# Optimization experiments

Measured on AMD Instinct MI355X. Metric: run time of the kernel, lower is better.

The kernel has to match this reference:

```python
import jax, jax.numpy as jnp
import numpy as np

DIM = 256
HEADS = 8
KS = 3          # deform conv kernel size
N = KS * KS     # sampling points per output pixel
PAD = 1


def conv2d(x, w, b=None, stride=1, padding=0):
    out = jax.lax.conv_general_dilated(
        x, w, (stride, stride), [(padding, padding)] * 2,
        dimension_numbers=('NCHW', 'OIHW', 'NCHW'))
    if b is not None:
        out = out + b[None, :, None, None]
    return out


def deform_conv(x, w_pconv, b_pconv, w_dconv):
    b, c, h, w = x.shape
    offset = conv2d(x, w_pconv, b_pconv, padding=1)      # (b, 2N, h, w)
    off = offset.transpose(0, 2, 3, 1)                   # (b, h, w, 2N); [:N]=x-off, [N:]=y-off
    xp = jnp.pad(x, ((0, 0), (0, 0), (PAD, PAD), (PAD, PAD)))
    hp, wp = h + 2 * PAD, w + 2 * PAD
    r = jnp.arange(-(KS - 1) // 2, (KS - 1) // 2 + 1, dtype=x.dtype)
    pnx, pny = jnp.meshgrid(r, r, indexing='ij')
    # sampling positions, 1-indexed into the padded input (matches the torch ref)
    px = off[..., :N] + pnx.reshape(-1) + jnp.arange(1, h + 1, dtype=x.dtype)[None, :, None, None]
    py = off[..., N:] + pny.reshape(-1) + jnp.arange(1, w + 1, dtype=x.dtype)[None, None, :, None]
    fx = jnp.floor(px)
    fy = jnp.floor(py)
    qlt_x = jnp.clip(fx, 0, hp - 1)
    qlt_y = jnp.clip(fy, 0, wp - 1)
    qrb_x = jnp.clip(fx + 1, 0, hp - 1)
    qrb_y = jnp.clip(fy + 1, 0, wp - 1)
    pxc = jnp.clip(px, 0, hp - 1)
    pyc = jnp.clip(py, 0, wp - 1)
    # bilinear weights (can be negative at clamped borders, as in the torch ref)
    g_lt = (1 + (qlt_x - pxc)) * (1 + (qlt_y - pyc))
    g_rb = (1 - (qrb_x - pxc)) * (1 - (qrb_y - pyc))
    g_lb = (1 + (qlt_x - pxc)) * (1 - (qrb_y - pyc))
    g_rt = (1 - (qrb_x - pxc)) * (1 + (qlt_y - pyc))
    ilt_x = qlt_x.astype(jnp.int32)
    ilt_y = qlt_y.astype(jnp.int32)
    irb_x = qrb_x.astype(jnp.int32)
    irb_y = qrb_y.astype(jnp.int32)

    def gather(xb, ix, iy):
        return xb[:, ix, iy]                              # (c, h, w, N)

    gat = jax.vmap(gather)
    x_lt = gat(xp, ilt_x, ilt_y)
    x_rb = gat(xp, irb_x, irb_y)
    x_lb = gat(xp, ilt_x, irb_y)
    x_rt = gat(xp, irb_x, ilt_y)
    x_off = (g_lt[:, None] * x_lt + g_rb[:, None] * x_rb
             + g_lb[:, None] * x_lb + g_rt[:, None] * x_rt)   # (b, c, h, w, N)
    # 'b c h w (i j) -> b c (h i) (w j)' then ks-strided conv
    x_off = x_off.reshape(b, c, h, w, KS, KS).transpose(0, 1, 2, 4, 3, 5)
    x_off = x_off.reshape(b, c, h * KS, w * KS)
    return conv2d(x_off, w_dconv, None, stride=KS)


def ssa_forward(x, w_pconv, b_pconv, w_dconv, w_qkv, temperature, w_proj):
    b, c, h, w = x.shape
    hw = h * w
    ch = c // HEADS
    q = deform_conv(x, w_pconv, b_pconv, w_dconv)         # (b, c, h, w)
    qkv = jnp.einsum('bchw,oc->bohw', x, w_qkv)           # 1x1 conv, (b, 3c, h, w)
    k = qkv[:, c:2 * c]
    v = qkv[:, 2 * c:]
    q = q.reshape(b, HEADS, ch, hw)
    k = k.reshape(b, HEADS, ch, hw)
    v = v.reshape(b, HEADS, ch, hw)
    k = k / jnp.maximum(jnp.linalg.norm(k, axis=-1, keepdims=True), 1e-12)
    v = v / jnp.maximum(jnp.linalg.norm(v, axis=-1, keepdims=True), 1e-12)
    attn = jnp.einsum('bhcn,bhdn->bhcd', q, k) * temperature[None]   # (b, h, ch, ch)
    attn = jax.nn.softmax(attn, axis=-1)
    out = jnp.einsum('bhcd,bhdn->bhcn', attn, v).reshape(b, c, h, w)
    return jnp.einsum('bchw,oc->bohw', out, w_proj)       # project_out 1x1


def setup_inputs() -> dict:
    key = jax.random.key(0)
    ks = jax.random.split(key, 6)
    B, H, W = 2, 96, 96
    x = jax.random.normal(ks[0], (B, DIM, H, W), jnp.float32)
    w_pconv = jax.random.normal(ks[1], (2 * N, DIM, KS, KS), jnp.float32) * 0.01
    b_pconv = jax.random.normal(ks[2], (2 * N,), jnp.float32) * 0.01
    w_dconv = jax.random.normal(ks[3], (DIM, DIM, KS, KS), jnp.float32) * 0.02
    w_qkv = jax.random.normal(ks[4], (3 * DIM, DIM), jnp.float32) * 0.05
    temperature = jnp.ones((HEADS, 1, 1), jnp.float32)
    w_proj = jax.random.normal(ks[5], (DIM, DIM), jnp.float32) * 0.05
    return dict(x=x, w_pconv=w_pconv, b_pconv=b_pconv, w_dconv=w_dconv,
                w_qkv=w_qkv, temperature=temperature, w_proj=w_proj)


def reference(x, w_pconv, b_pconv, w_dconv, w_qkv, temperature, w_proj):
    return ssa_forward(x, w_pconv, b_pconv, w_dconv, w_qkv, temperature, w_proj)
```

## Files before the change

### kernel.cpp

```cpp
#include <hip/hip_runtime.h>
#include <math.h>

#define BB 2
#define CC 256
#define HW 96
#define PP 9216
#define KO 18
#define HEADS 8
#define NCH 18

typedef short bf16x8 __attribute__((ext_vector_type(8)));
typedef float f32x4 __attribute__((ext_vector_type(4)));

#define NP_O    0UL
#define W2_O    147456UL
#define IDX_O   331776UL
#define WGT_O   995328UL
#define WT2_O   1658880UL
#define WP2_O   2248704UL
#define WQ2_O   2322432UL
#define QP_O    2584576UL
#define KV_O    12021760UL
#define AP_O    21459968UL

__device__ __forceinline__ ushort f2bf_rne(float f) {
    unsigned u = __float_as_uint(f);
    unsigned r = (u + 0x7FFFu + ((u >> 16) & 1u)) >> 16;
    return (ushort)r;
}
__device__ __forceinline__ float bf2f(ushort h) {
    return __uint_as_float(((unsigned)h) << 16);
}

__global__ __launch_bounds__(256) void k_prep_wt(const float* __restrict__ wd,
                                                 ushort* __restrict__ h,
                                                 ushort* __restrict__ lo) {
    int tid = blockIdx.x * 256 + threadIdx.x;
    if (tid >= 9 * 8 * 1024 * 8) return;
    int e = tid & 7;
    int u = (tid >> 3) & 1023;
    int cs = (tid >> 13) & 7;
    int kk = tid >> 16;
    int oh = u >> 6, rem = u & 63;
    int lrow = rem & 15, lhi = rem >> 4;
    int o = oh * 16 + lrow;
    int c = cs * 32 + lhi * 8 + e;
    float v = wd[o * 2304 + c * 9 + kk];
    ushort hh = f2bf_rne(v);
    h[tid] = hh;
    lo[tid] = f2bf_rne(v - bf2f(hh));
}

__global__ __launch_bounds__(256) void k_prep_wp(const float* __restrict__ wp,
                                                 ushort* __restrict__ h,
                                                 ushort* __restrict__ lo) {
    int tid = blockIdx.x * 256 + threadIdx.x;
    if (tid >= 9 * 8 * 128 * 8) return;
    int e = tid & 7;
    int u = (tid >> 3) & 127;
    int cs = (tid >> 10) & 7;
    int kk = tid >> 13;
    int mf = u >> 6, rem = u & 63;
    int lrow = rem & 15, lhi = rem >> 4;
    int o = mf * 16 + lrow;
    int c = cs * 32 + lhi * 8 + e;
    float v = (o < KO) ? wp[(o * 256 + c) * 9 + kk] : 0.f;
    ushort hh = f2bf_rne(v);
    h[tid] = hh;
    lo[tid] = f2bf_rne(v - bf2f(hh));
}

__global__ __launch_bounds__(256) void k_prep_w(const float* __restrict__ W,
                                                ushort* __restrict__ h,
                                                ushort* __restrict__ lo,
                                                int total) {
    int tid = blockIdx.x * 256 + threadIdx.x;
    if (tid >= total) return;
    int e = tid & 7;
    int u = (tid >> 3) & 1023;
    int csg = (tid >> 13) & 7;
    int mt = tid >> 16;
    int rem = u & 63;
    int lrow = rem & 15, lhi = rem >> 4;
    int o = mt * 256 + (u >> 6) * 16 + lrow;
    int c = csg * 32 + lhi * 8 + e;
    float v = W[o * 256 + c];
    ushort hh = f2bf_rne(v);
    h[tid] = hh;
    lo[tid] = f2bf_rne(v - bf2f(hh));
}

__global__ __launch_bounds__(256) void k_pconv(const float* __restrict__ x,
                                               const ushort* __restrict__ wp2h,
                                               const ushort* __restrict__ wp2l,
                                               float* __restrict__ ppart) {
    int s = blockIdx.x;
    int xcd = s & 7;
    int b = xcd & 1, ks = xcd >> 1;
    int p0 = (s >> 3) * 64;
    int t = threadIdx.x;
    int l = t & 63, w = t >> 6;
    int lrow = l & 15, lhi = l >> 4;
    int p = t & 63, cg = t >> 6;
    __shared__ __align__(16) ushort Sh[64 * 40];
    __shared__ __align__(16) ushort Sl[64 * 40];
    f32x4 acc[2];
    acc[0] = (f32x4)0.f; acc[1] = (f32x4)0.f;
    const float* xb = x + (size_t)b * CC * PP;
    int pix = p0 + p;
    int i_ = pix / 96, j_ = pix % 96;
#pragma unroll 1
    for (int cs = 0; cs < 2; ++cs) {
        int csg = ks * 2 + cs;
        const float* xc0 = xb + (size_t)(csg * 32 + cg * 8) * PP;
#pragma unroll 1
        for (int kk = 0; kk < 9; ++kk) {
            int di = kk / 3 - 1, dj = kk % 3 - 1;
            bool vOK = ((unsigned)(i_ + di) < 96u) && ((unsigned)(j_ + dj) < 96u);
            int poff = pix + di * 96 + dj;
            __syncthreads();
            bf16x8 ah[2], al[2];
#pragma unroll
            for (int mf = 0; mf < 2; ++mf) {
                size_t gi = (((size_t)(kk * 8 + csg)) * 128 + (mf * 64 + l)) * 8;
                ah[mf] = *(const bf16x8*)&wp2h[gi];
                al[mf] = *(const bf16x8*)&wp2l[gi];
            }
            bf16x8 vh, vl;
#pragma unroll
            for (int i = 0; i < 8; ++i) {
                float v = vOK ? xc0[(size_t)i * PP + poff] : 0.f;
                ushort hh = f2bf_rne(v);
                vh[i] = (short)hh;
                vl[i] = (short)f2bf_rne(v - bf2f(hh));
            }
            *(bf16x8*)&Sh[p * 40 + cg * 8] = vh;
            *(bf16x8*)&Sl[p * 40 + cg * 8] = vl;
            __syncthreads();
            bf16x8 Bh = *(const bf16x8*)&Sh[(w * 16 + lrow) * 40 + lhi * 8];
            bf16x8 Bl = *(const bf16x8*)&Sl[(w * 16 + lrow) * 40 + lhi * 8];
#pragma unroll
            for (int mf = 0; mf < 2; ++mf) {
                acc[mf] = __builtin_amdgcn_mfma_f32_16x16x32_bf16(ah[mf], Bh, acc[mf], 0, 0, 0);
                acc[mf] = __builtin_amdgcn_mfma_f32_16x16x32_bf16(ah[mf], Bl, acc[mf], 0, 0, 0);
                acc[mf] = __builtin_amdgcn_mfma_f32_16x16x32_bf16(al[mf], Bh, acc[mf], 0, 0, 0);
            }
        }
    }
    float* pr = ppart + ((size_t)(ks * BB + b) * 32) * PP;
#pragma unroll
    for (int mf = 0; mf < 2; ++mf)
#pragma unroll
        for (int j = 0; j < 4; ++j)
            pr[(size_t)(mf * 16 + lhi * 4 + j) * PP + p0 + w * 16 + lrow] = acc[mf][j];
}

__global__ __launch_bounds__(256) void k_bilin2(const float* __restrict__ pp,
                                                const float* __restrict__ bp,
                                                int4* __restrict__ idx4,
                                                float4* __restrict__ wgt4) {
    int idx = blockIdx.x * 256 + threadIdx.x;
    if (idx >= BB * 9 * PP) return;
    int p = idx % PP;
    int bn = idx / PP;
    int n = bn % 9, b = bn / 9;
    int i = p / 96, j = p % 96;
    float ox = bp[n], oy = bp[n + 9];
#pragma unroll
    for (int k = 0; k < 4; ++k) {
        ox += pp[((size_t)(k * BB + b) * 32 + n) * PP + p];
        oy += pp[((size_t)(k * BB + b) * 32 + n + 9) * PP + p];
    }
    float px = ox + (float)(n / 3 - 1) + (float)(i + 1);
    float py = oy + (float)(n % 3 - 1) + (float)(j + 1);
    float fx = floorf(px), fy = floorf(py);
    float qltx = fminf(fmaxf(fx, 0.f), 97.f);
    float qlty = fminf(fmaxf(fy, 0.f), 97.f);
    float qrbx = fminf(fmaxf(fx + 1.f, 0.f), 97.f);
    float qrby = fminf(fmaxf(fy + 1.f, 0.f), 97.f);
    float pxc = fminf(fmaxf(px, 0.f), 97.f);
    float pyc = fminf(fmaxf(py, 0.f), 97.f);
    float glt = (1.f + (qltx - pxc)) * (1.f + (qlty - pyc));
    float grb = (1.f - (qrbx - pxc)) * (1.f - (qrby - pyc));
    float glb = (1.f + (qltx - pxc)) * (1.f - (qrby - pyc));
    float grt = (1.f - (qrbx - pxc)) * (1.f + (qlty - pyc));
    int x0 = (int)qltx - 1, y0 = (int)qlty - 1;
    int x1 = (int)qrbx - 1, y1 = (int)qrby - 1;
    bool vlt = (x0 >= 0 && x0 < 96 && y0 >= 0 && y0 < 96);
    bool vrb = (x1 >= 0 && x1 < 96 && y1 >= 0 && y1 < 96);
    bool vlb = (x0 >= 0 && x0 < 96 && y1 >= 0 && y1 < 96);
    bool vrt = (x1 >= 0 && x1 < 96 && y0 >= 0 && y0 < 96);
    int4 id;
    id.x = vlt ? x0 * 96 + y0 : 0;
    id.y = vrb ? x1 * 96 + y1 : 0;
    id.z = vlb ? x0 * 96 + y1 : 0;
    id.w = vrt ? x1 * 96 + y0 : 0;
    idx4[idx] = id;
    wgt4[idx] = make_float4(vlt ? glt : 0.f, vrb ? grb : 0.f,
                            vlb ? glb : 0.f, vrt ? grt : 0.f);
}

__global__ __launch_bounds__(256) void k_dconv(const float* __restrict__ x,
                                               const ushort* __restrict__ wt2h,
                                               const ushort* __restrict__ wt2l,
                                               const int4* __restrict__ idx4,
                                               const float4* __restrict__ wgt4,
                                               float* __restrict__ qpart) {
    int s = blockIdx.x;
    int xcd = s & 7, ib = s >> 3;
    int combo = xcd >> 1;
    int b = combo & 1;
    int half = combo >> 1;
    int ptile = (xcd & 1) * 144 + ib;
    int p0 = ptile * 32;
    int t = threadIdx.x;
    int l = t & 63, w = t >> 6;
    int lrow = l & 15, lhi = l >> 4;
    int obase = w * 64;
    int pl = t & 31, cg = t >> 5;

    __shared__ __align__(16) ushort Sh0[32 * 40], Sl0[32 * 40];
    __shared__ __align__(16) ushort Sh1[32 * 40], Sl1[32 * 40];
    __shared__ int4 Tid[9 * 32];
    __shared__ float4 Twg[9 * 32];

    for (int e = t; e < 9 * 32; e += 256) {
        int kk = e >> 5, pq = e & 31;
        size_t tb = ((size_t)b * 9 + kk) * PP + p0 + pq;
        Tid[e] = idx4[tb];
        Twg[e] = wgt4[tb];
    }

    f32x4 acc[4][2];
#pragma unroll
    for (int mf = 0; mf < 4; ++mf)
#pragma unroll
        for (int nf = 0; nf < 2; ++nf) acc[mf][nf] = (f32x4)0.f;

    const float* xb = x + (size_t)b * CC * PP;
    int h4 = half * 4;

    float R[16];
    float4 g4r;

    auto LD = [&](int i) {
        int cs = i / 9, kk = i % 9;
        int csg = h4 + cs;
        int4 id = Tid[kk * 32 + pl];
        g4r = Twg[kk * 32 + pl];
        const float* xp0 = xb + (size_t)(csg * 32 + cg * 4) * PP;
#pragma unroll
        for (int q = 0; q < 4; ++q) {
            const float* xc = xp0 + (size_t)q * PP;
            R[q * 4 + 0] = xc[id.x];
            R[q * 4 + 1] = xc[id.y];
            R[q * 4 + 2] = xc[id.z];
            R[q * 4 + 3] = xc[id.w];
        }
    };
    auto CONV = [&](ushort* Sh, ushort* Sl) {
        ushort4 vh, vl;
#pragma unroll
        for (int q = 0; q < 4; ++q) {
            float v = g4r.x * R[q * 4 + 0];
            v = fmaf(g4r.y, R[q * 4 + 1], v);
            v = fmaf(g4r.z, R[q * 4 + 2], v);
            v = fmaf(g4r.w, R[q * 4 + 3], v);
            ushort hh = f2bf_rne(v);
            ushort ll = f2bf_rne(v - bf2f(hh));
            if (q == 0)      { vh.x = hh; vl.x = ll; }
            else if (q == 1) { vh.y = hh; vl.y = ll; }
            else if (q == 2) { vh.z = hh; vl.z = ll; }
            else             { vh.w = hh; vl.w = ll; }
        }
        *(ushort4*)&Sh[pl * 40 + cg * 4] = vh;
        *(ushort4*)&Sl[pl * 40 + cg * 4] = vl;
    };
    auto COMPUTE = [&](int i, const ushort* Sh, const ushort* Sl) {
        int cs = i / 9, kk = i % 9;
        int csg = h4 + cs;
        bf16x8 ah[4], al[4];
#pragma unroll
        for (int mf = 0; mf < 4; ++mf) {
            size_t gi = (((size_t)(kk * 8 + csg)) * 1024 + ((w * 4 + mf) * 64 + l)) * 8;
            ah[mf] = *(const bf16x8*)&wt2h[gi];
            al[mf] = *(const bf16x8*)&wt2l[gi];
        }
        bf16x8 Bh2[2], Bl2[2];
#pragma unroll
        for (int nf = 0; nf < 2; ++nf) {
            Bh2[nf] = *(const bf16x8*)&Sh[(nf * 16 + lrow) * 40 + lhi * 8];
            Bl2[nf] = *(const bf16x8*)&Sl[(nf * 16 + lrow) * 40 + lhi * 8];
        }
        __builtin_amdgcn_s_setprio(1);
#pragma unroll
        for (int mf = 0; mf < 4; ++mf)
#pragma unroll
            for (int nf = 0; nf < 2; ++nf) {
                acc[mf][nf] = __builtin_amdgcn_mfma_f32_16x16x32_bf16(ah[mf], Bh2[nf], acc[mf][nf], 0, 0, 0);
                acc[mf][nf] = __builtin_amdgcn_mfma_f32_16x16x32_bf16(ah[mf], Bl2[nf], acc[mf][nf], 0, 0, 0);
                acc[mf][nf] = __builtin_amdgcn_mfma_f32_16x16x32_bf16(al[mf], Bh2[nf], acc[mf][nf], 0, 0, 0);
            }
        __builtin_amdgcn_s_setprio(0);
    };

    __syncthreads();
    LD(0); CONV(Sh0, Sl0);
    LD(1);
    __syncthreads();

#pragma unroll 1
    for (int i0 = 0; i0 < 36; i0 += 2) {
        CONV(Sh1, Sl1);
        if (i0 + 2 < 36) LD(i0 + 2);
        COMPUTE(i0, Sh0, Sl0);
        __syncthreads();
        if (i0 + 2 < 36) CONV(Sh0, Sl0);
        if (i0 + 3 < 36) LD(i0 + 3);
        COMPUTE(i0 + 1, Sh1, Sl1);
        __syncthreads();
    }

    float* qh = qpart + (size_t)half * BB * CC * PP + (size_t)b * CC * PP;
#pragma unroll
    for (int mf = 0; mf < 4; ++mf)
#pragma unroll
        for (int nf = 0; nf < 2; ++nf)
#pragma unroll
            for (int j = 0; j < 4; ++j)
                qh[(size_t)(obase + mf * 16 + lhi * 4 + j) * PP + p0 + nf * 16 + lrow] =
                    acc[mf][nf][j];
}

__global__ __launch_bounds__(256) void k_gemm_bf(const float* __restrict__ Bsrc,
                                                 const ushort* __restrict__ A2h,
                                                 const ushort* __restrict__ A2l,
                                                 float* __restrict__ C,
                                                 int mtiles, int bRowStride, int bRowOff,
                                                 int aBatchStride,
                                                 float* __restrict__ npart) {
    int s = blockIdx.x;
    int xcd = s & 7, ib = s >> 3;
    int b, mt, ptile;
    if (mtiles == 2) {
        int combo = xcd >> 1;
        b = combo & 1; mt = combo >> 1;
        ptile = (xcd & 1) * 72 + ib;
    } else {
        b = xcd >> 2; mt = 0;
        ptile = (xcd & 3) * 36 + ib;
    }
    int p0 = ptile * 64;
    int t = threadIdx.x;
    int l = t & 63, w = t >> 6;
    int lrow = l & 15, lhi = l >> 4;
    int obase = w * 64;
    int p = t & 63, cg = t >> 6;
    __shared__ __align__(16) ushort Sh[64 * 40];
    __shared__ __align__(16) ushort Sl[64 * 40];
    f32x4 acc[4][4];
#pragma unroll
    for (int mf = 0; mf < 4; ++mf)
#pragma unroll
        for (int nf = 0; nf < 4; ++nf) acc[mf][nf] = (f32x4)0.f;
    const float* Bb = Bsrc + ((size_t)b * bRowStride + bRowOff) * PP;
    const ushort* Ah = A2h + (size_t)b * aBatchStride;
    const ushort* Al = A2l + (size_t)b * aBatchStride;
#pragma unroll 1
    for (int csg = 0; csg < 8; ++csg) {
        __syncthreads();
        bf16x8 ah[4], al[4];
#pragma unroll
        for (int mf = 0; mf < 4; ++mf) {
            size_t gi = (((size_t)(mt * 8 + csg)) * 1024 + ((w * 4 + mf) * 64 + l)) * 8;
            ah[mf] = *(const bf16x8*)&Ah[gi];
            al[mf] = *(const bf16x8*)&Al[gi];
        }
        const float* xr = Bb + (size_t)(csg * 32 + cg * 8) * PP + p0 + p;
        bf16x8 vh, vl;
#pragma unroll
        for (int i = 0; i < 8; ++i) {
            float v = xr[(size_t)i * PP];
            ushort hh = f2bf_rne(v);
            vh[i] = (short)hh;
            vl[i] = (short)f2bf_rne(v - bf2f(hh));
        }
        *(bf16x8*)&Sh[p * 40 + cg * 8] = vh;
        *(bf16x8*)&Sl[p * 40 + cg * 8] = vl;
        __syncthreads();
        bf16x8 Bh4[4], Bl4[4];
#pragma unroll
        for (int nf = 0; nf < 4; ++nf) {
            Bh4[nf] = *(const bf16x8*)&Sh[(nf * 16 + lrow) * 40 + lhi * 8];
            Bl4[nf] = *(const bf16x8*)&Sl[(nf * 16 + lrow) * 40 + lhi * 8];
        }
#pragma unroll
        for (int mf = 0; mf < 4; ++mf) {
#pragma unroll
            for (int nf = 0; nf < 4; ++nf) {
                acc[mf][nf] = __builtin_amdgcn_mfma_f32_16x16x32_bf16(ah[mf], Bh4[nf], acc[mf][nf], 0, 0, 0);
                acc[mf][nf] = __builtin_amdgcn_mfma_f32_16x16x32_bf16(ah[mf], Bl4[nf], acc[mf][nf], 0, 0, 0);
                acc[mf][nf] = __builtin_amdgcn_mfma_f32_16x16x32_bf16(al[mf], Bh4[nf], acc[mf][nf], 0, 0, 0);
            }
        }
    }
    float* Cb = C + (size_t)b * (mtiles * 256) * PP;
#pragma unroll
    for (int mf = 0; mf < 4; ++mf)
#pragma unroll
        for (int nf = 0; nf < 4; ++nf)
#pragma unroll
            for (int j = 0; j < 4; ++j)
                Cb[(size_t)(mt * 256 + obase + mf * 16 + lhi * 4 + j) * PP + p0 + nf * 16 + lrow] =
                    acc[mf][nf][j];
    if (npart) {
        float sq[4][4];
#pragma unroll
        for (int mf = 0; mf < 4; ++mf)
#pragma unroll
            for (int j = 0; j < 4; ++j) {
                float v0 = acc[mf][0][j], v1 = acc[mf][1][j];
                float v2 = acc[mf][2][j], v3 = acc[mf][3][j];
                sq[mf][j] = v0 * v0 + v1 * v1 + v2 * v2 + v3 * v3;
            }
#pragma unroll
        for (int m = 1; m <= 8; m <<= 1)
#pragma unroll
            for (int mf = 0; mf < 4; ++mf)
#pragma unroll
                for (int j = 0; j < 4; ++j)
                    sq[mf][j] += __shfl_xor(sq[mf][j], m, 64);
        if (lrow == 0) {
            float* np = npart + ((size_t)(b * 2 + mt) * 144 + ptile) * 256;
#pragma unroll
            for (int mf = 0; mf < 4; ++mf)
#pragma unroll
                for (int j = 0; j < 4; ++j)
                    np[obase + mf * 16 + lhi * 4 + j] = sq[mf][j];
        }
    }
}

__global__ __launch_bounds__(256) void k_attn_part(const float* __restrict__ qp,
                                                   const float* __restrict__ kv,
                                                   float* __restrict__ apart) {
    int ch = blockIdx.x, h = blockIdx.y, b = blockIdx.z;
    int t = threadIdx.x;
    int d = t & 31, cg = t >> 5;
    __shared__ float qs[32][37], ks[32][37];
    float acc[4] = {0.f, 0.f, 0.f, 0.f};
    const float* q0 = qp + ((size_t)b * CC + h * 32) * PP;
    const float* q1 = q0 + (size_t)BB * CC * PP;
    const float* kb = kv + ((size_t)b * 512 + h * 32) * PP;
    int r = t >> 3, cq = (t & 7) * 4;
    for (int po = ch * 512; po < ch * 512 + 512; po += 32) {
        float4 va = *(const float4*)&q0[(size_t)r * PP + po + cq];
        float4 vb = *(const float4*)&q1[(size_t)r * PP + po + cq];
        qs[r][cq + 0] = va.x + vb.x; qs[r][cq + 1] = va.y + vb.y;
        qs[r][cq + 2] = va.z + vb.z; qs[r][cq + 3] = va.w + vb.w;
        float4 vk = *(const float4*)&kb[(size_t)r * PP + po + cq];
        ks[r][cq + 0] = vk.x; ks[r][cq + 1] = vk.y;
        ks[r][cq + 2] = vk.z; ks[r][cq + 3] = vk.w;
        __syncthreads();
#pragma unroll
        for (int pq = 0; pq < 32; ++pq) {
            float kvv = ks[d][pq];
#pragma unroll
            for (int i = 0; i < 4; ++i)
                acc[i] = fmaf(qs[cg * 4 + i][pq], kvv, acc[i]);
        }
        __syncthreads();
    }
    float* ap = apart + (((size_t)(b * 8 + h) * NCH + ch) << 10);
#pragma unroll
    for (int i = 0; i < 4; ++i) ap[(cg * 4 + i) * 32 + d] = acc[i];
}

__global__ __launch_bounds__(256) void k_attn_fin_w2(const float* __restrict__ apart,
                                                     const float* __restrict__ npart,
                                                     const float* __restrict__ temp,
                                                     const float* __restrict__ wproj,
                                                     ushort* __restrict__ w2h,
                                                     ushort* __restrict__ w2l) {
    int h = blockIdx.x, b = blockIdx.y;
    int t = threadIdx.x;
    __shared__ float A[32][33];
    __shared__ float invk[32], invv[32];
    if (t < 64) {
        int mt = t >> 5, row = (t & 31) + h * 32;
        const float* base = npart + ((size_t)(b * 2 + mt) * 144) * 256 + row;
        float ssum = 0.f;
        for (int pt = 0; pt < 144; ++pt) ssum += base[pt * 256];
        float iv = 1.f / fmaxf(sqrtf(ssum), 1e-12f);
        if (mt == 0) invk[t & 31] = iv; else invv[t & 31] = iv;
    }
    const float* ap = apart + ((size_t)(b * 8 + h) * NCH << 10);
    float th = temp[h];
    for (int e = t; e < 1024; e += 256) {
        float s = 0.f;
        for (int chn = 0; chn < NCH; ++chn) s += ap[chn * 1024 + e];
        A[e >> 5][e & 31] = s * th;
    }
    __syncthreads();
    if (t < 32) {
        int c = t;
        float m = -INFINITY;
        float row[32];
#pragma unroll
        for (int d = 0; d < 32; ++d) {
            row[d] = A[c][d] * invk[d];
            m = fmaxf(m, row[d]);
        }
        float sum = 0.f;
#pragma unroll
        for (int d = 0; d < 32; ++d) sum += expf(row[d] - m);
        float inv = 1.f / sum;
#pragma unroll
        for (int d = 0; d < 32; ++d)
            A[c][d] = expf(row[d] - m) * inv * invv[d];
    }
    __syncthreads();
    int o = t;
    float wrow[32];
#pragma unroll
    for (int c = 0; c < 32; ++c) wrow[c] = wproj[o * 256 + h * 32 + c];
    int wq = o >> 6, mf = (o >> 4) & 3, lr = o & 15;
    size_t bb = (size_t)b * 65536;
#pragma unroll
    for (int e = 0; e < 32; ++e) {
        float v = 0.f;
#pragma unroll
        for (int c = 0; c < 32; ++c) v = fmaf(wrow[c], A[c][e], v);
        int lhi = e >> 3, ee = e & 7;
        size_t gi = bb + ((size_t)h * 1024 + ((wq * 4 + mf) * 64 + lhi * 16 + lr)) * 8 + ee;
        ushort hh = f2bf_rne(v);
        w2h[gi] = hh;
        w2l[gi] = f2bf_rne(v - bf2f(hh));
    }
}

extern "C" void kernel_launch(void* const* d_in, const int* in_sizes, int n_in,
                              void* d_out, int out_size, void* d_ws, size_t ws_size,
                              hipStream_t stream) {
    const float* x     = (const float*)d_in[0];
    const float* wp    = (const float*)d_in[1];
    const float* bp    = (const float*)d_in[2];
    const float* wd    = (const float*)d_in[3];
    const float* wqkv  = (const float*)d_in[4];
    const float* temp  = (const float*)d_in[5];
    const float* wproj = (const float*)d_in[6];
    float* out = (float*)d_out;
    float* ws  = (float*)d_ws;

    float* npart  = ws + NP_O;
    ushort* w2h   = (ushort*)(ws + W2_O);
    ushort* w2l   = w2h + 2 * 65536;
    int4*  idx4   = (int4*)(ws + IDX_O);
    float4* wgt4  = (float4*)(ws + WGT_O);
    ushort* wt2h  = (ushort*)(ws + WT2_O);
    ushort* wt2l  = wt2h + 9 * 8 * 1024 * 8;
    ushort* wp2h  = (ushort*)(ws + WP2_O);
    ushort* wp2l  = wp2h + 9 * 8 * 128 * 8;
    ushort* wq2h  = (ushort*)(ws + WQ2_O);
    ushort* wq2l  = wq2h + 2 * 8 * 1024 * 8;
    float* qpart  = ws + QP_O;
    float* ppart  = ws + QP_O;
    float* kv     = ws + KV_O;
    float* apart  = ws + AP_O;

    k_prep_wt<<<2304, 256, 0, stream>>>(wd, wt2h, wt2l);
    k_prep_wp<<<288, 256, 0, stream>>>(wp, wp2h, wp2l);
    k_prep_w<<<512, 256, 0, stream>>>(wqkv + 256 * 256, wq2h, wq2l, 2 * 65536);
    k_pconv<<<1152, 256, 0, stream>>>(x, wp2h, wp2l, ppart);
    k_bilin2<<<(BB * 9 * PP + 255) / 256, 256, 0, stream>>>(ppart, bp, idx4, wgt4);
    k_dconv<<<1152, 256, 0, stream>>>(x, wt2h, wt2l, idx4, wgt4, qpart);
    k_gemm_bf<<<576, 256, 0, stream>>>(x, wq2h, wq2l, kv, 2, 256, 0, 0, npart);
    k_attn_part<<<dim3(NCH, HEADS, BB), 256, 0, stream>>>(qpart, kv, apart);
    k_attn_fin_w2<<<dim3(HEADS, BB), 256, 0, stream>>>(apart, npart, temp, wproj, w2h, w2l);
    k_gemm_bf<<<288, 256, 0, stream>>>(kv, w2h, w2l, out, 1, 512, 256, 65536, nullptr);
}
```

Measured before the change: 300.5 us.

## Transpose input to pixel-major layout so deform-conv gathers load float4 channel vectors

```diff
diff --git a/kernel.cpp b/kernel.cpp
--- a/kernel.cpp
+++ b/kernel.cpp
@@ -88,6 +88,36 @@
     ushort hh = f2bf_rne(v);
     h[tid] = hh;
     lo[tid] = f2bf_rne(v - bf2f(hh));
+}
+
+__global__ __launch_bounds__(256) void k_xt(const float* __restrict__ x,
+                                            float* __restrict__ xT) {
+    int pt = blockIdx.x;
+    int ct = blockIdx.y;
+    int b  = blockIdx.z;
+    int t = threadIdx.x;
+    __shared__ float T[64][65];
+    {
+        int c = t >> 2, pq = (t & 3) * 16;
+        const float* src = x + ((size_t)b * CC + ct * 64 + c) * PP + pt * 64 + pq;
+#pragma unroll
+        for (int k2 = 0; k2 < 4; ++k2) {
+            float4 v = *(const float4*)&src[k2 * 4];
+            T[c][pq + k2 * 4 + 0] = v.x;
+            T[c][pq + k2 * 4 + 1] = v.y;
+            T[c][pq + k2 * 4 + 2] = v.z;
+            T[c][pq + k2 * 4 + 3] = v.w;
+        }
+    }
+    __syncthreads();
+    {
+        int p = t >> 2, cq = (t & 3) * 16;
+        float* dst = xT + ((size_t)b * PP + pt * 64 + p) * CC + ct * 64 + cq;
+#pragma unroll
+        for (int k2 = 0; k2 < 4; ++k2)
+            *(float4*)&dst[k2 * 4] = make_float4(T[cq + k2 * 4 + 0][p], T[cq + k2 * 4 + 1][p],
+                                                 T[cq + k2 * 4 + 2][p], T[cq + k2 * 4 + 3][p]);
+    }
 }
 
 __global__ __launch_bounds__(256) void k_pconv(const float* __restrict__ x,
@@ -200,7 +230,7 @@
                             vlb ? glb : 0.f, vrt ? grt : 0.f);
 }
 
-__global__ __launch_bounds__(256) void k_dconv(const float* __restrict__ x,
+__global__ __launch_bounds__(256) void k_dconv(const float* __restrict__ xT,
                                                const ushort* __restrict__ wt2h,
                                                const ushort* __restrict__ wt2l,
                                                const int4* __restrict__ idx4,
@@ -237,7 +267,7 @@
 #pragma unroll
         for (int nf = 0; nf < 2; ++nf) acc[mf][nf] = (f32x4)0.f;
 
-    const float* xb = x + (size_t)b * CC * PP;
+    const float* xTb = xT + (size_t)b * PP * CC;
     int h4 = half * 4;
 
     float R[16];
@@ -248,24 +278,20 @@
         int csg = h4 + cs;
         int4 id = Tid[kk * 32 + pl];
         g4r = Twg[kk * 32 + pl];
-        const float* xp0 = xb + (size_t)(csg * 32 + cg * 4) * PP;
-#pragma unroll
-        for (int q = 0; q < 4; ++q) {
-            const float* xc = xp0 + (size_t)q * PP;
-            R[q * 4 + 0] = xc[id.x];
-            R[q * 4 + 1] = xc[id.y];
-            R[q * 4 + 2] = xc[id.z];
-            R[q * 4 + 3] = xc[id.w];
-        }
+        const float* xt0 = xTb + (size_t)(csg * 32 + cg * 4);
+        *(float4*)&R[0]  = *(const float4*)&xt0[(size_t)id.x * CC];
+        *(float4*)&R[4]  = *(const float4*)&xt0[(size_t)id.y * CC];
+        *(float4*)&R[8]  = *(const float4*)&xt0[(size_t)id.z * CC];
+        *(float4*)&R[12] = *(const float4*)&xt0[(size_t)id.w * CC];
     };
     auto CONV = [&](ushort* Sh, ushort* Sl) {
         ushort4 vh, vl;
 #pragma unroll
         for (int q = 0; q < 4; ++q) {
-            float v = g4r.x * R[q * 4 + 0];
-            v = fmaf(g4r.y, R[q * 4 + 1], v);
-            v = fmaf(g4r.z, R[q * 4 + 2], v);
-            v = fmaf(g4r.w, R[q * 4 + 3], v);
+            float v = g4r.x * R[q];
+            v = fmaf(g4r.y, R[4 + q], v);
+            v = fmaf(g4r.z, R[8 + q], v);
+            v = fmaf(g4r.w, R[12 + q], v);
             ushort hh = f2bf_rne(v);
             ushort ll = f2bf_rne(v - bf2f(hh));
             if (q == 0)      { vh.x = hh; vl.x = ll; }
@@ -565,6 +591,7 @@
     ushort* wq2l  = wq2h + 2 * 8 * 1024 * 8;
     float* qpart  = ws + QP_O;
     float* ppart  = ws + QP_O;
+    float* xT     = ws + KV_O;
     float* kv     = ws + KV_O;
     float* apart  = ws + AP_O;
 
@@ -573,7 +600,8 @@
     k_prep_w<<<512, 256, 0, stream>>>(wqkv + 256 * 256, wq2h, wq2l, 2 * 65536);
     k_pconv<<<1152, 256, 0, stream>>>(x, wp2h, wp2l, ppart);
     k_bilin2<<<(BB * 9 * PP + 255) / 256, 256, 0, stream>>>(ppart, bp, idx4, wgt4);
-    k_dconv<<<1152, 256, 0, stream>>>(x, wt2h, wt2l, idx4, wgt4, qpart);
+    k_xt<<<dim3(144, 4, BB), 256, 0, stream>>>(x, xT);
+    k_dconv<<<1152, 256, 0, stream>>>(xT, wt2h, wt2l, idx4, wgt4, qpart);
     k_gemm_bf<<<576, 256, 0, stream>>>(x, wq2h, wq2l, kv, 2, 256, 0, 0, npart);
     k_attn_part<<<dim3(NCH, HEADS, BB), 256, 0, stream>>>(qpart, kv, apart);
     k_attn_fin_w2<<<dim3(HEADS, BB), 256, 0, stream>>>(apart, npart, temp, wproj, w2h, w2l);
```

New measurement: 267.3 us. 11.1% less time.
